# Optimization experiments

Measured on AMD Instinct MI355X. Metric: run time of the kernel, lower is better.

The kernel has to match this reference:

```python
import jax, jax.numpy as jnp
import numpy as np

DEPTH_K = 64
DEPTH_V = 64
NUM_HEADS = 8


def setup_inputs() -> dict:
    key = jax.random.key(0)
    k1, k2, k3 = jax.random.split(key, 3)
    B, H, W = 2, 48, 48
    C = 2 * DEPTH_K + DEPTH_V  # 192
    dkh = DEPTH_K // NUM_HEADS  # 8
    inputs = jax.random.normal(k1, (B, H, W, C), dtype=jnp.float32)
    # RandomNormal(stddev=dkh**-0.5) initializer
    key_rel_w = jax.random.normal(k2, (2 * W - 1, dkh), dtype=jnp.float32) * dkh ** (-0.5)
    key_rel_h = jax.random.normal(k3, (2 * H - 1, dkh), dtype=jnp.float32) * dkh ** (-0.5)
    return {"inputs": inputs, "key_rel_w": key_rel_w, "key_rel_h": key_rel_h}


def rel_to_abs(x):
    # x: [B, N, L, 2L-1] -> [B, N, L, L] via the pad/reshape skew trick
    B, N, L, _ = x.shape
    x = jnp.pad(x, ((0, 0), (0, 0), (0, 0), (0, 1)))          # [B,N,L,2L]
    flat = x.reshape(B, N, L * 2 * L)
    flat = jnp.pad(flat, ((0, 0), (0, 0), (0, L - 1)))
    final = flat.reshape(B, N, L + 1, 2 * L - 1)
    return final[:, :, :L, L - 1:]


def rel_logits_1d(q, rel_k, transpose_mask):
    # q: [B, nh, H, W, d]; rel_k: [2W-1, d]
    B, nh, H, W, d = q.shape
    rl = jnp.einsum('bhxyd,md->bhxym', q, rel_k)              # [B,nh,H,W,2W-1]
    rl = rel_to_abs(rl.reshape(B, nh * H, W, 2 * W - 1))      # [B,nh*H,W,W]
    rl = rl.reshape(B, nh, H, W, W)
    rl = jnp.broadcast_to(rl[:, :, :, None, :, :], (B, nh, H, H, W, W))
    rl = jnp.transpose(rl, transpose_mask)
    return rl.reshape(B, nh, H * W, H * W)


def attention_augmentation_2d(inputs, key_rel_w, key_rel_h):
    B, H, W, C = inputs.shape
    nh = NUM_HEADS
    dkh = DEPTH_K // nh
    dvh = DEPTH_V // nh
    q, k, v = jnp.split(inputs, [DEPTH_K, 2 * DEPTH_K], axis=-1)

    def split_heads(x):
        d = x.shape[-1] // nh
        return jnp.transpose(x.reshape(B, H, W, nh, d), (0, 3, 1, 2, 4))  # [B,nh,H,W,d]

    q = split_heads(q) * dkh ** (-0.5)
    k = split_heads(k)
    v = split_heads(v)

    flat_q = q.reshape(B, nh, H * W, dkh)
    flat_k = k.reshape(B, nh, H * W, dkh)
    flat_v = v.reshape(B, nh, H * W, dvh)

    logits = jnp.einsum('bhnd,bhmd->bhnm', flat_q, flat_k)    # [B,nh,HW,HW]
    # relative logits: width uses q as-is, height uses q with H/W swapped
    w_rel = rel_logits_1d(q, key_rel_w, (0, 1, 2, 4, 3, 5))
    h_rel = rel_logits_1d(jnp.transpose(q, (0, 1, 3, 2, 4)), key_rel_h, (0, 1, 4, 2, 5, 3))
    logits = logits + h_rel + w_rel

    weights = jax.nn.softmax(logits, axis=-1)
    attn = jnp.einsum('bhnm,bhmd->bhnd', weights, flat_v)     # [B,nh,HW,dvh]
    attn = attn.reshape(B, nh, H, W, dvh)
    out = jnp.transpose(attn, (0, 2, 3, 1, 4)).reshape(B, H, W, DEPTH_V)
    return out


def reference(inputs, key_rel_w, key_rel_h):
    return attention_augmentation_2d(inputs, key_rel_w, key_rel_h)
```

## Files before the change

kernel.cpp:

```cpp
#include <hip/hip_runtime.h>
#include <stdint.h>

#define WW 48
#define NQ 2304
#define NWT 144
#define SCL 0.51011868f
#define SHIFT 17.312340491f
#define ACCF (NWT * 2304)
#define QHF (16 * 48 * 2304)

typedef float v2f __attribute__((ext_vector_type(2)));

__device__ __forceinline__ v2f v2fma(v2f a, v2f b, v2f c) {
    return __builtin_elementwise_fma(a, b, c);
}

__global__ __launch_bounds__(256) void qh_pre(const float* __restrict__ in,
                                              const float* __restrict__ relh,
                                              float* __restrict__ QH,
                                              float* __restrict__ ACC) {
    const int bx = blockIdx.x;
    const int seg = bx / NWT;
    const int wt = bx - seg * NWT;
    float* ab = ACC + (size_t)wt * 2304 + seg * 576;
    for (int i = threadIdx.x; i < 576; i += 256) ab[i] = 0.0f;

    const int bh = wt / 9;
    const int nt = wt - bh * 9;
    const int n = nt * 256 + threadIdx.x;
    const int b = bh >> 3, h = bh & 7;
    const int y = n / WW;

    const float* qp = in + ((size_t)(b * NQ + n) * 192 + h * 8);
    float4 a = *(const float4*)qp, bb = *(const float4*)(qp + 4);
    v2f Q0 = {a.x * SCL, a.y * SCL}, Q1 = {a.z * SCL, a.w * SCL};
    v2f Q2 = {bb.x * SCL, bb.y * SCL}, Q3 = {bb.z * SCL, bb.w * SCL};

    const int y2end = seg * 12 + 12;
    for (int y2 = seg * 12; y2 < y2end; ++y2) {
        const float* rh = relh + (y2 - y + 47) * 8;
        float4 ta = *(const float4*)rh, tb = *(const float4*)(rh + 4);
        v2f s = v2fma(Q0, (v2f){ta.x, ta.y},
                v2fma(Q1, (v2f){ta.z, ta.w},
                v2fma(Q2, (v2f){tb.x, tb.y},
                      Q3 * (v2f){tb.z, tb.w})));
        QH[(size_t)(bh * 48 + y2) * 2304 + n] = s.x + s.y - SHIFT;
    }
}

__global__ __launch_bounds__(256, 2) void attn_kernel(const float* __restrict__ in,
                                                      const float* __restrict__ relw,
                                                      const float* __restrict__ QH,
                                                      float* __restrict__ ACC) {
    __shared__ float4 lds[1152];

    const int bx = blockIdx.x;
    const int wt = bx % NWT;
    const int gg = bx / NWT;
    const int bh = wt / 9;
    const int qt = wt - bh * 9;
    const int tid = threadIdx.x;
    const int lane = tid & 63;
    const int wv = tid >> 6;
    const int kc = gg;
    const int b = bh >> 3, h = bh & 7;

    const float4* inp4 = (const float4*)in;
    for (int t = tid; t < 576; t += 256) {
        const int key = t >> 2, p = t & 3;
        const int row = key / 3, col = key - row * 3;
        const size_t px = (size_t)(b * NQ + row * 48 + kc * 3 + col) * 48;
        const int c4 = (p < 2) ? (16 + h * 2 + p) : (32 + h * 2 + (p - 2));
        lds[t] = inp4[px + c4];
    }

    v2f Q0[4], Q1[4], Q2[4], Q3[4];
    int xq[4];
#pragma unroll
    for (int j = 0; j < 4; ++j) {
        const int n = qt * 256 + j * 64 + lane;
        const int y = n / WW;
        xq[j] = n - y * WW;
        const float* qp = in + ((size_t)(b * NQ + n) * 192 + h * 8);
        float4 a = *(const float4*)qp, bb = *(const float4*)(qp + 4);
        Q0[j] = (v2f){a.x * SCL, a.y * SCL};
        Q1[j] = (v2f){a.z * SCL, a.w * SCL};
        Q2[j] = (v2f){bb.x * SCL, bb.y * SCL};
        Q3[j] = (v2f){bb.z * SCL, bb.w * SCL};
    }

    float qw[4][3];
#pragma unroll
    for (int j = 0; j < 4; ++j)
#pragma unroll
        for (int c = 0; c < 3; ++c) {
            const float* rw = relw + (kc * 3 + c - xq[j] + 47) * 8;
            float4 ta = *(const float4*)rw, tb = *(const float4*)(rw + 4);
            v2f s = v2fma(Q0[j], (v2f){ta.x, ta.y},
                    v2fma(Q1[j], (v2f){ta.z, ta.w},
                    v2fma(Q2[j], (v2f){tb.x, tb.y},
                          Q3[j] * (v2f){tb.z, tb.w})));
            qw[j][c] = s.x + s.y;
        }

    __syncthreads();

    float l[4] = {0, 0, 0, 0};
    v2f A0[4], A1[4], A2[4], A3[4];
#pragma unroll
    for (int j = 0; j < 4; ++j) {
        A0[j] = (v2f){0.f, 0.f}; A1[j] = (v2f){0.f, 0.f};
        A2[j] = (v2f){0.f, 0.f}; A3[j] = (v2f){0.f, 0.f};
    }
    const float* myl = (const float*)lds;
    const float* qhbase = QH + (size_t)bh * 48 * 2304 + qt * 256 + lane;

#pragma unroll 1
    for (int R = 0; R < 3; ++R) {
        float qh[4][4];
#pragma unroll
        for (int row = 0; row < 4; ++row) {
            const int y2 = wv * 12 + R * 4 + row;
            const float* qr = qhbase + (size_t)y2 * 2304;
#pragma unroll
            for (int j = 0; j < 4; ++j) qh[j][row] = qr[j * 64];
        }

#pragma unroll 2
        for (int row = 0; row < 4; ++row) {
            const int y2 = wv * 12 + R * 4 + row;
#pragma unroll
            for (int c = 0; c < 3; ++c) {
                const int base = (y2 * 3 + c) * 16;
                const float4 k0 = *(const float4*)(myl + base);
                const float4 k1 = *(const float4*)(myl + base + 4);
                const float4 v0 = *(const float4*)(myl + base + 8);
                const float4 v1 = *(const float4*)(myl + base + 12);
                const v2f K0 = {k0.x, k0.y}, K1 = {k0.z, k0.w};
                const v2f K2 = {k1.x, k1.y}, K3 = {k1.z, k1.w};
                const v2f V0 = {v0.x, v0.y}, V1 = {v0.z, v0.w};
                const v2f V2 = {v1.x, v1.y}, V3 = {v1.z, v1.w};
#pragma unroll
                for (int j = 0; j < 4; ++j) {
                    v2f d = v2fma(Q0[j], K0,
                            v2fma(Q1[j], K1,
                            v2fma(Q2[j], K2, Q3[j] * K3)));
                    const float p = __builtin_amdgcn_exp2f(
                        (qh[j][row] + qw[j][c]) + (d.x + d.y));
                    l[j] += p;
                    const v2f pp = {p, p};
                    A0[j] = v2fma(pp, V0, A0[j]);
                    A1[j] = v2fma(pp, V1, A1[j]);
                    A2[j] = v2fma(pp, V2, A2[j]);
                    A3[j] = v2fma(pp, V3, A3[j]);
                }
            }
        }
    }

    __syncthreads();
    float* mr = (float*)(lds + (wv >> 1) * 576);
    if ((wv & 1) == 0) {
#pragma unroll
        for (int j = 0; j < 4; ++j) {
            const int q = j * 64 + lane;
            mr[q] = l[j];
            mr[1 * 256 + q] = A0[j].x; mr[2 * 256 + q] = A0[j].y;
            mr[3 * 256 + q] = A1[j].x; mr[4 * 256 + q] = A1[j].y;
            mr[5 * 256 + q] = A2[j].x; mr[6 * 256 + q] = A2[j].y;
            mr[7 * 256 + q] = A3[j].x; mr[8 * 256 + q] = A3[j].y;
        }
    }
    __syncthreads();
    if ((wv & 1) == 1) {
#pragma unroll
        for (int j = 0; j < 4; ++j) {
            const int q = j * 64 + lane;
            mr[q] += l[j];
            mr[1 * 256 + q] += A0[j].x; mr[2 * 256 + q] += A0[j].y;
            mr[3 * 256 + q] += A1[j].x; mr[4 * 256 + q] += A1[j].y;
            mr[5 * 256 + q] += A2[j].x; mr[6 * 256 + q] += A2[j].y;
            mr[7 * 256 + q] += A3[j].x; mr[8 * 256 + q] += A3[j].y;
        }
    }
    __syncthreads();

    const float* r0 = (const float*)lds;
    const float* r1 = (const float*)(lds + 576);
    float* ab = ACC + (size_t)wt * 2304;
    for (int idx = tid; idx < 2304; idx += 256)
        atomicAdd(ab + idx, r0[idx] + r1[idx]);
}

__global__ __launch_bounds__(64) void norm_kernel(const float* __restrict__ ACC,
                                                  float* __restrict__ out) {
    const int bxx = blockIdx.x;
    const int wt = bxx >> 2;
    const int q = (bxx & 3) * 64 + threadIdx.x;
    const float* ab = ACC + (size_t)wt * 2304;
    const float inv = 1.0f / ab[q];
    float s[8];
#pragma unroll
    for (int e = 0; e < 8; ++e) s[e] = ab[(1 + e) * 256 + q] * inv;
    const int bh = wt / 9;
    const int qtl = wt - bh * 9;
    const int n = qtl * 256 + q;
    const int b = bh >> 3, h = bh & 7;
    float* op = out + ((size_t)(b * NQ + n) * 64 + h * 8);
    ((float4*)op)[0] = make_float4(s[0], s[1], s[2], s[3]);
    ((float4*)op)[1] = make_float4(s[4], s[5], s[6], s[7]);
}

extern "C" void kernel_launch(void* const* d_in, const int* in_sizes, int n_in,
                              void* d_out, int out_size, void* d_ws, size_t ws_size,
                              hipStream_t stream) {
    const float* in   = (const float*)d_in[0];
    const float* relw = (const float*)d_in[1];
    const float* relh = (const float*)d_in[2];
    float* ACC = (float*)d_ws;
    float* QH  = (float*)d_ws + ACCF;
    float* out = (float*)d_out;

    qh_pre<<<4 * NWT, 256, 0, stream>>>(in, relh, QH, ACC);
    attn_kernel<<<16 * NWT, 256, 0, stream>>>(in, relw, QH, ACC);
    norm_kernel<<<4 * NWT, 64, 0, stream>>>(ACC, out);
}
```

Measured before the change: 128.0 us.

## Fuse height relative-logit computation into attention kernel, drop precompute pass

Removes the qh_pre kernel, which wrote a precomputed height-relative logit table to global memory. The attention kernel now stages the key_rel_h table in LDS and recomputes each query's height logit per row with a short dot product, and the shift constant moves into the width term. The ACC buffer is now zeroed with hipMemsetAsync instead of inside the old kernel. This removes one launch and the global write and read of the QH table, at the cost of extra FMAs and LDS reads in the inner loop plus a little more shared memory.

```diff
diff --git a/kernel.cpp b/kernel.cpp
--- a/kernel.cpp
+++ b/kernel.cpp
@@ -7,7 +7,6 @@
 #define SCL 0.51011868f
 #define SHIFT 17.312340491f
 #define ACCF (NWT * 2304)
-#define QHF (16 * 48 * 2304)
 
 typedef float v2f __attribute__((ext_vector_type(2)));
 
@@ -15,44 +14,11 @@
     return __builtin_elementwise_fma(a, b, c);
 }
 
-__global__ __launch_bounds__(256) void qh_pre(const float* __restrict__ in,
-                                              const float* __restrict__ relh,
-                                              float* __restrict__ QH,
-                                              float* __restrict__ ACC) {
-    const int bx = blockIdx.x;
-    const int seg = bx / NWT;
-    const int wt = bx - seg * NWT;
-    float* ab = ACC + (size_t)wt * 2304 + seg * 576;
-    for (int i = threadIdx.x; i < 576; i += 256) ab[i] = 0.0f;
-
-    const int bh = wt / 9;
-    const int nt = wt - bh * 9;
-    const int n = nt * 256 + threadIdx.x;
-    const int b = bh >> 3, h = bh & 7;
-    const int y = n / WW;
-
-    const float* qp = in + ((size_t)(b * NQ + n) * 192 + h * 8);
-    float4 a = *(const float4*)qp, bb = *(const float4*)(qp + 4);
-    v2f Q0 = {a.x * SCL, a.y * SCL}, Q1 = {a.z * SCL, a.w * SCL};
-    v2f Q2 = {bb.x * SCL, bb.y * SCL}, Q3 = {bb.z * SCL, bb.w * SCL};
-
-    const int y2end = seg * 12 + 12;
-    for (int y2 = seg * 12; y2 < y2end; ++y2) {
-        const float* rh = relh + (y2 - y + 47) * 8;
-        float4 ta = *(const float4*)rh, tb = *(const float4*)(rh + 4);
-        v2f s = v2fma(Q0, (v2f){ta.x, ta.y},
-                v2fma(Q1, (v2f){ta.z, ta.w},
-                v2fma(Q2, (v2f){tb.x, tb.y},
-                      Q3 * (v2f){tb.z, tb.w})));
-        QH[(size_t)(bh * 48 + y2) * 2304 + n] = s.x + s.y - SHIFT;
-    }
-}
-
 __global__ __launch_bounds__(256, 2) void attn_kernel(const float* __restrict__ in,
                                                       const float* __restrict__ relw,
-                                                      const float* __restrict__ QH,
+                                                      const float* __restrict__ relh,
                                                       float* __restrict__ ACC) {
-    __shared__ float4 lds[1152];
+    __shared__ float4 lds[1342];
 
     const int bx = blockIdx.x;
     const int wt = bx % NWT;
@@ -73,14 +39,16 @@
         const int c4 = (p < 2) ? (16 + h * 2 + p) : (32 + h * 2 + (p - 2));
         lds[t] = inp4[px + c4];
     }
+    for (int t = tid; t < 190; t += 256) lds[1152 + t] = ((const float4*)relh)[t];
 
     v2f Q0[4], Q1[4], Q2[4], Q3[4];
-    int xq[4];
+    int xq[4], ro[4];
 #pragma unroll
     for (int j = 0; j < 4; ++j) {
         const int n = qt * 256 + j * 64 + lane;
         const int y = n / WW;
         xq[j] = n - y * WW;
+        ro[j] = (47 - y) * 8;
         const float* qp = in + ((size_t)(b * NQ + n) * 192 + h * 8);
         float4 a = *(const float4*)qp, bb = *(const float4*)(qp + 4);
         Q0[j] = (v2f){a.x * SCL, a.y * SCL};
@@ -100,7 +68,7 @@
                     v2fma(Q1[j], (v2f){ta.z, ta.w},
                     v2fma(Q2[j], (v2f){tb.x, tb.y},
                           Q3[j] * (v2f){tb.z, tb.w})));
-            qw[j][c] = s.x + s.y;
+            qw[j][c] = s.x + s.y - SHIFT;
         }
 
     __syncthreads();
@@ -113,22 +81,25 @@
         A2[j] = (v2f){0.f, 0.f}; A3[j] = (v2f){0.f, 0.f};
     }
     const float* myl = (const float*)lds;
-    const float* qhbase = QH + (size_t)bh * 48 * 2304 + qt * 256 + lane;
+    const float* relh_lds = (const float*)(lds + 1152);
 
 #pragma unroll 1
     for (int R = 0; R < 3; ++R) {
-        float qh[4][4];
-#pragma unroll
-        for (int row = 0; row < 4; ++row) {
-            const int y2 = wv * 12 + R * 4 + row;
-            const float* qr = qhbase + (size_t)y2 * 2304;
-#pragma unroll
-            for (int j = 0; j < 4; ++j) qh[j][row] = qr[j * 64];
-        }
-
 #pragma unroll 2
         for (int row = 0; row < 4; ++row) {
             const int y2 = wv * 12 + R * 4 + row;
+            float qhv[4];
+#pragma unroll
+            for (int j = 0; j < 4; ++j) {
+                const float* rp = relh_lds + ro[j] + y2 * 8;
+                const float4 ra = *(const float4*)rp;
+                const float4 rb = *(const float4*)(rp + 4);
+                v2f s = v2fma(Q0[j], (v2f){ra.x, ra.y},
+                        v2fma(Q1[j], (v2f){ra.z, ra.w},
+                        v2fma(Q2[j], (v2f){rb.x, rb.y},
+                              Q3[j] * (v2f){rb.z, rb.w})));
+                qhv[j] = s.x + s.y;
+            }
 #pragma unroll
             for (int c = 0; c < 3; ++c) {
                 const int base = (y2 * 3 + c) * 16;
@@ -146,7 +117,7 @@
                             v2fma(Q1[j], K1,
                             v2fma(Q2[j], K2, Q3[j] * K3)));
                     const float p = __builtin_amdgcn_exp2f(
-                        (qh[j][row] + qw[j][c]) + (d.x + d.y));
+                        (qhv[j] + qw[j][c]) + (d.x + d.y));
                     l[j] += p;
                     const v2f pp = {p, p};
                     A0[j] = v2fma(pp, V0, A0[j]);
@@ -218,10 +189,9 @@
     const float* relw = (const float*)d_in[1];
     const float* relh = (const float*)d_in[2];
     float* ACC = (float*)d_ws;
-    float* QH  = (float*)d_ws + ACCF;
     float* out = (float*)d_out;
 
-    qh_pre<<<4 * NWT, 256, 0, stream>>>(in, relh, QH, ACC);
-    attn_kernel<<<16 * NWT, 256, 0, stream>>>(in, relw, QH, ACC);
+    hipMemsetAsync(ACC, 0, ACCF * sizeof(float), stream);
+    attn_kernel<<<16 * NWT, 256, 0, stream>>>(in, relw, relh, ACC);
     norm_kernel<<<4 * NWT, 64, 0, stream>>>(ACC, out);
 }
```

After: 120.7 us. -5.7%, faster.
